# Kernel tuning notes

Measured on AMD Instinct MI355X. Metric: run time of the kernel, lower is better.

The kernel has to match this reference:

```python
import jax, jax.numpy as jnp
import numpy as np

N_NODES = 100000
N_EDGES = 800000
N_GRAPHS = 512
C_IN = 32
N_CLASSES = 10


def setup_inputs() -> dict:
    key = jax.random.key(0)
    ks = jax.random.split(key, 12)
    x = jax.random.normal(ks[0], (N_NODES, C_IN), dtype=jnp.float32)
    edge_index = jax.random.randint(ks[1], (2, N_EDGES), 0, N_NODES, dtype=jnp.int64)
    batch = jnp.sort(jax.random.randint(ks[2], (N_NODES,), 0, N_GRAPHS, dtype=jnp.int64))
    # GCNConv weights initialized ~ N(0, 1/sqrt(in_channels)) per the source
    W1 = jax.random.normal(ks[3], (C_IN, 64), dtype=jnp.float32) / np.sqrt(C_IN).astype(np.float32)
    bc1 = jnp.zeros((64,), jnp.float32)
    W2 = jax.random.normal(ks[4], (64, 128), dtype=jnp.float32) / np.sqrt(64).astype(np.float32)
    bc2 = jnp.zeros((128,), jnp.float32)
    W3 = jax.random.normal(ks[5], (128, 256), dtype=jnp.float32) / np.sqrt(128).astype(np.float32)
    bc3 = jnp.zeros((256,), jnp.float32)
    Wlin = jnp.full((256, N_CLASSES), 0.01, jnp.float32)  # lin.weight filled with 0.01
    blin = jnp.zeros((N_CLASSES,), jnp.float32)
    return dict(x=x, edge_index=edge_index, batch=batch,
                W1=W1, bc1=bc1, W2=W2, bc2=bc2, W3=W3, bc3=bc3,
                Wlin=Wlin, blin=blin)


def _gcn_conv(x, W, b, src, dst, n_nodes):
    """PyG GCNConv: symmetric-normalized aggregation with self-loops.
    out = D^{-1/2} (A + I) D^{-1/2} (x W) + b
    """
    h = x @ W  # [N, F_out]
    ones_e = jnp.ones(src.shape, h.dtype)
    deg = jax.ops.segment_sum(ones_e, dst, num_segments=n_nodes) + 1.0  # self-loop included
    dinv = jax.lax.rsqrt(deg)
    norm = dinv[src] * dinv[dst]  # [E]
    agg = jax.ops.segment_sum(h[src] * norm[:, None], dst, num_segments=n_nodes)
    # self-loop contribution: norm_ii = dinv_i^2
    return agg + h * (dinv * dinv)[:, None] + b


def reference(x, edge_index, batch, W1, bc1, W2, bc2, W3, bc3, Wlin, blin):
    src, dst = edge_index[0], edge_index[1]
    h = jax.nn.relu(_gcn_conv(x, W1, bc1, src, dst, N_NODES))
    h = jax.nn.relu(_gcn_conv(h, W2, bc2, src, dst, N_NODES))
    h = _gcn_conv(h, W3, bc3, src, dst, N_NODES)  # no relu before pooling (matches source)
    # global mean pool over graphs
    summed = jax.ops.segment_sum(h, batch, num_segments=N_GRAPHS)  # [G, 256]
    counts = jax.ops.segment_sum(jnp.ones((N_NODES, 1), h.dtype), batch, num_segments=N_GRAPHS)
    pooled = summed / jnp.clip(counts, 1.0)
    return pooled @ Wlin + blin  # [G, num_classes]
```

## Files before the change

kernel.cpp:

```cpp
#include <hip/hip_runtime.h>
#include <hip/hip_bf16.h>


#define NN 100000
#define NE 800000
#define NG 512
#define PARTS 4

typedef unsigned int u32;

__device__ __forceinline__ u32 pack_bf2(float lo, float hi) {
    u32 ul = __float_as_uint(lo);
    u32 uh = __float_as_uint(hi);
    ul = (ul + 0x7fffu + ((ul >> 16) & 1u)) >> 16;
    uh = (uh + 0x7fffu + ((uh >> 16) & 1u)) & 0xffff0000u;
    return uh | ul;
}

#define BF_FMA8(ACC, V, W_) do { \
    (ACC)[0] += __uint_as_float((V).x << 16) * (W_); \
    (ACC)[1] += __uint_as_float((V).x & 0xffff0000u) * (W_); \
    (ACC)[2] += __uint_as_float((V).y << 16) * (W_); \
    (ACC)[3] += __uint_as_float((V).y & 0xffff0000u) * (W_); \
    (ACC)[4] += __uint_as_float((V).z << 16) * (W_); \
    (ACC)[5] += __uint_as_float((V).z & 0xffff0000u) * (W_); \
    (ACC)[6] += __uint_as_float((V).w << 16) * (W_); \
    (ACC)[7] += __uint_as_float((V).w & 0xffff0000u) * (W_); \
} while (0)

#define FMA4(A, H, W_) do { (A).x += (H).x * (W_); (A).y += (H).y * (W_); \
                            (A).z += (H).z * (W_); (A).w += (H).w * (W_); } while (0)

__global__ __launch_bounds__(256) void deg_count(const int* __restrict__ dst,
                                                 int* __restrict__ deg, int nE) {
    int e = blockIdx.x * 256 + threadIdx.x;
    if (e < nE) atomicAdd(&deg[dst[e]], 1);
}

__global__ __launch_bounds__(256) void scanA(const int* __restrict__ deg,
                                             int* __restrict__ ex,
                                             int* __restrict__ bsum, int n) {
    __shared__ int sdata[256];
    const int t = threadIdx.x;
    const int base = blockIdx.x * 1024;
    const int idx = base + t * 4;
    int v[4];
#pragma unroll
    for (int k = 0; k < 4; ++k) v[k] = (idx + k < n) ? deg[idx + k] : 0;
    int ts = v[0] + v[1] + v[2] + v[3];
    sdata[t] = ts;
    __syncthreads();
    for (int off = 1; off < 256; off <<= 1) {
        int val = (t >= off) ? sdata[t - off] : 0;
        __syncthreads();
        sdata[t] += val;
        __syncthreads();
    }
    int run = sdata[t] - ts;
    if (t == 255) bsum[blockIdx.x] = sdata[255];
#pragma unroll
    for (int k = 0; k < 4; ++k) {
        if (idx + k < n) ex[idx + k] = run;
        run += v[k];
    }
}

__global__ __launch_bounds__(128) void scanB(int* __restrict__ bsum, int nb) {
    __shared__ int s[128];
    const int t = threadIdx.x;
    int orig = (t < nb) ? bsum[t] : 0;
    s[t] = orig;
    __syncthreads();
    for (int off = 1; off < 128; off <<= 1) {
        int val = (t >= off) ? s[t - off] : 0;
        __syncthreads();
        s[t] += val;
        __syncthreads();
    }
    if (t < nb) bsum[t] = s[t] - orig;
}

__global__ __launch_bounds__(256) void scanC(int* __restrict__ rp,
                                             const int* __restrict__ bsum,
                                             int* __restrict__ cursor,
                                             const int* __restrict__ deg,
                                             float* __restrict__ dinv,
                                             int n, int total) {
    int i = blockIdx.x * 256 + threadIdx.x;
    if (i < n) {
        int v = rp[i] + bsum[i >> 10];
        rp[i] = v;
        cursor[i] = v;
        dinv[i] = rsqrtf((float)deg[i] + 1.0f);
    }
    if (i == n) rp[n] = total;
}

__global__ __launch_bounds__(256) void fill_csr(const int* __restrict__ ei,
                                                const float* __restrict__ dinv,
                                                int* __restrict__ cursor,
                                                int2* __restrict__ cw, int nE) {
    int e = blockIdx.x * 256 + threadIdx.x;
    if (e >= nE) return;
    const int s = ei[e];
    const int d = ei[nE + e];
    const int pos = atomicAdd(&cursor[d], 1);
    const float wv = dinv[s] * dinv[d];
    cw[pos] = make_int2(s, __float_as_int(wv));
}

__global__ __launch_bounds__(256) void gather_gemm_l1(const float* __restrict__ X,
                                                      const int* __restrict__ rp,
                                                      const int2* __restrict__ cw,
                                                      const float* __restrict__ dinv,
                                                      const float* __restrict__ W,
                                                      const float* __restrict__ bias,
                                                      u32* __restrict__ out, int n) {
    constexpr int AS = 36;
    __shared__ float agg[32 * AS];
    __shared__ float Wl[32 * 64];
    float4 wr[2];
#pragma unroll
    for (int i = 0; i < 2; ++i)
        wr[i] = *reinterpret_cast<const float4*>(&W[(threadIdx.x + i * 256) * 4]);

    const int nl = threadIdx.x >> 3;
    const int j = (threadIdx.x & 7) * 4;
    const int node = blockIdx.x * 32 + nl;
    float4 a0 = make_float4(0.f, 0.f, 0.f, 0.f);
    float4 a1 = a0, a2 = a0, a3 = a0;
    if (node < n) {
        const float di = dinv[node];
        const float c = di * di;
        const float4 sv = *reinterpret_cast<const float4*>(&X[(long long)node * 32 + j]);
        FMA4(a0, sv, c);
        int e = rp[node];
        const int end = rp[node + 1];
        for (; e + 4 <= end; e += 4) {
            const int2 c0 = cw[e], c1 = cw[e + 1], c2 = cw[e + 2], c3 = cw[e + 3];
            const float4 h0 = *reinterpret_cast<const float4*>(&X[(long long)c0.x * 32 + j]);
            const float4 h1 = *reinterpret_cast<const float4*>(&X[(long long)c1.x * 32 + j]);
            const float4 h2 = *reinterpret_cast<const float4*>(&X[(long long)c2.x * 32 + j]);
            const float4 h3 = *reinterpret_cast<const float4*>(&X[(long long)c3.x * 32 + j]);
            FMA4(a0, h0, __int_as_float(c0.y));
            FMA4(a1, h1, __int_as_float(c1.y));
            FMA4(a2, h2, __int_as_float(c2.y));
            FMA4(a3, h3, __int_as_float(c3.y));
        }
        if (e + 2 <= end) {
            const int2 c0 = cw[e], c1 = cw[e + 1];
            const float4 h0 = *reinterpret_cast<const float4*>(&X[(long long)c0.x * 32 + j]);
            const float4 h1 = *reinterpret_cast<const float4*>(&X[(long long)c1.x * 32 + j]);
            FMA4(a0, h0, __int_as_float(c0.y));
            FMA4(a1, h1, __int_as_float(c1.y));
            e += 2;
        }
        if (e < end) {
            const int2 c0 = cw[e];
            const float4 h0 = *reinterpret_cast<const float4*>(&X[(long long)c0.x * 32 + j]);
            FMA4(a0, h0, __int_as_float(c0.y));
        }
        a0.x += a1.x + a2.x + a3.x; a0.y += a1.y + a2.y + a3.y;
        a0.z += a1.z + a2.z + a3.z; a0.w += a1.w + a2.w + a3.w;
    }
    *reinterpret_cast<float4*>(&agg[nl * AS + j]) = a0;
#pragma unroll
    for (int i = 0; i < 2; ++i)
        *reinterpret_cast<float4*>(&Wl[(threadIdx.x + i * 256) * 4]) = wr[i];
    __syncthreads();

    const int r0 = (threadIdx.x >> 4) * 2;
    const int cg = (threadIdx.x & 15) * 4;
    float4 o0 = make_float4(0.f, 0.f, 0.f, 0.f);
    float4 o1 = o0;
#pragma unroll 8
    for (int k = 0; k < 32; ++k) {
        const float4 wv = *reinterpret_cast<const float4*>(&Wl[k * 64 + cg]);
        const float x0 = agg[r0 * AS + k];
        const float x1 = agg[(r0 + 1) * AS + k];
        FMA4(o0, wv, x0);
        FMA4(o1, wv, x1);
    }
    const float4 bv = *reinterpret_cast<const float4*>(&bias[cg]);
    o0.x = fmaxf(o0.x + bv.x, 0.f); o0.y = fmaxf(o0.y + bv.y, 0.f);
    o0.z = fmaxf(o0.z + bv.z, 0.f); o0.w = fmaxf(o0.w + bv.w, 0.f);
    o1.x = fmaxf(o1.x + bv.x, 0.f); o1.y = fmaxf(o1.y + bv.y, 0.f);
    o1.z = fmaxf(o1.z + bv.z, 0.f); o1.w = fmaxf(o1.w + bv.w, 0.f);
    const int row0 = blockIdx.x * 32 + r0;
    if (row0 < n)
        *reinterpret_cast<uint2*>(&out[(long long)row0 * 32 + (cg >> 1)]) =
            make_uint2(pack_bf2(o0.x, o0.y), pack_bf2(o0.z, o0.w));
    if (row0 + 1 < n)
        *reinterpret_cast<uint2*>(&out[(long long)(row0 + 1) * 32 + (cg >> 1)]) =
            make_uint2(pack_bf2(o1.x, o1.y), pack_bf2(o1.z, o1.w));
}

__global__ __launch_bounds__(256) void gather_gemm_l2(const u32* __restrict__ X,
                                                      const int* __restrict__ rp,
                                                      const int2* __restrict__ cw,
                                                      const float* __restrict__ dinv,
                                                      const float* __restrict__ W,
                                                      const float* __restrict__ bias,
                                                      u32* __restrict__ out, int n) {
    constexpr int AS = 68;
    __shared__ float agg[32 * AS];
    __shared__ float Wl[64 * 128];
    float4 wr[8];
#pragma unroll
    for (int i = 0; i < 8; ++i)
        wr[i] = *reinterpret_cast<const float4*>(&W[(threadIdx.x + i * 256) * 4]);

    const int nl = threadIdx.x >> 3;
    const int j = threadIdx.x & 7;
    const int node = blockIdx.x * 32 + nl;
    float a0[8], a1[8], a2[8], a3[8];
#pragma unroll
    for (int q = 0; q < 8; ++q) { a0[q] = 0.f; a1[q] = 0.f; a2[q] = 0.f; a3[q] = 0.f; }
    if (node < n) {
        const float di = dinv[node];
        const float c = di * di;
        const uint4 sv = *reinterpret_cast<const uint4*>(&X[(long long)node * 32 + j * 4]);
        BF_FMA8(a0, sv, c);
        int e = rp[node];
        const int end = rp[node + 1];
        for (; e + 4 <= end; e += 4) {
            const int2 c0 = cw[e], c1 = cw[e + 1], c2 = cw[e + 2], c3 = cw[e + 3];
            const uint4 h0 = *reinterpret_cast<const uint4*>(&X[(long long)c0.x * 32 + j * 4]);
            const uint4 h1 = *reinterpret_cast<const uint4*>(&X[(long long)c1.x * 32 + j * 4]);
            const uint4 h2 = *reinterpret_cast<const uint4*>(&X[(long long)c2.x * 32 + j * 4]);
            const uint4 h3 = *reinterpret_cast<const uint4*>(&X[(long long)c3.x * 32 + j * 4]);
            BF_FMA8(a0, h0, __int_as_float(c0.y));
            BF_FMA8(a1, h1, __int_as_float(c1.y));
            BF_FMA8(a2, h2, __int_as_float(c2.y));
            BF_FMA8(a3, h3, __int_as_float(c3.y));
        }
        if (e + 2 <= end) {
            const int2 c0 = cw[e], c1 = cw[e + 1];
            const uint4 h0 = *reinterpret_cast<const uint4*>(&X[(long long)c0.x * 32 + j * 4]);
            const uint4 h1 = *reinterpret_cast<const uint4*>(&X[(long long)c1.x * 32 + j * 4]);
            BF_FMA8(a0, h0, __int_as_float(c0.y));
            BF_FMA8(a1, h1, __int_as_float(c1.y));
            e += 2;
        }
        if (e < end) {
            const int2 c0 = cw[e];
            const uint4 h0 = *reinterpret_cast<const uint4*>(&X[(long long)c0.x * 32 + j * 4]);
            BF_FMA8(a0, h0, __int_as_float(c0.y));
        }
#pragma unroll
        for (int q = 0; q < 8; ++q) a0[q] += a1[q] + a2[q] + a3[q];
    }
    *reinterpret_cast<float4*>(&agg[nl * AS + j * 8]) =
        make_float4(a0[0], a0[1], a0[2], a0[3]);
    *reinterpret_cast<float4*>(&agg[nl * AS + j * 8 + 4]) =
        make_float4(a0[4], a0[5], a0[6], a0[7]);
#pragma unroll
    for (int i = 0; i < 8; ++i)
        *reinterpret_cast<float4*>(&Wl[(threadIdx.x + i * 256) * 4]) = wr[i];
    __syncthreads();

    const int r0 = (threadIdx.x >> 5) * 4;
    const int cg = (threadIdx.x & 31) * 4;
    float4 o0 = make_float4(0.f, 0.f, 0.f, 0.f);
    float4 o1 = o0, o2 = o0, o3 = o0;
#pragma unroll 8
    for (int k = 0; k < 64; ++k) {
        const float4 wv = *reinterpret_cast<const float4*>(&Wl[k * 128 + cg]);
        const float x0 = agg[(r0 + 0) * AS + k];
        const float x1 = agg[(r0 + 1) * AS + k];
        const float x2 = agg[(r0 + 2) * AS + k];
        const float x3 = agg[(r0 + 3) * AS + k];
        FMA4(o0, wv, x0);
        FMA4(o1, wv, x1);
        FMA4(o2, wv, x2);
        FMA4(o3, wv, x3);
    }
    const float4 bv = *reinterpret_cast<const float4*>(&bias[cg]);
    const int row0 = blockIdx.x * 32 + r0;
    float4 oo[4] = {o0, o1, o2, o3};
#pragma unroll
    for (int r = 0; r < 4; ++r) {
        float4 o = oo[r];
        o.x = fmaxf(o.x + bv.x, 0.f); o.y = fmaxf(o.y + bv.y, 0.f);
        o.z = fmaxf(o.z + bv.z, 0.f); o.w = fmaxf(o.w + bv.w, 0.f);
        if (row0 + r < n)
            *reinterpret_cast<uint2*>(&out[(long long)(row0 + r) * 64 + (cg >> 1)]) =
                make_uint2(pack_bf2(o.x, o.y), pack_bf2(o.z, o.w));
    }
}

__device__ __forceinline__ int lower_bound_i(const int* __restrict__ a, int n, int key) {
    int lo = 0, hi = n;
    while (lo < hi) {
        int mid = (lo + hi) >> 1;
        if (a[mid] < key) lo = mid + 1; else hi = mid;
    }
    return lo;
}

__global__ __launch_bounds__(256) void gather_pool(const u32* __restrict__ H,
                                                   const int* __restrict__ rp,
                                                   const int2* __restrict__ cw,
                                                   const float* __restrict__ dinv,
                                                   const int* __restrict__ batch,
                                                   float* __restrict__ Spart, int n) {
    __shared__ float red[16 * 128];
    const int g = blockIdx.x / PARTS;
    const int part = blockIdx.x % PARTS;
    const int slot = threadIdx.x >> 4;
    const int j = threadIdx.x & 15;
    const int start = lower_bound_i(batch, n, g);
    const int end = lower_bound_i(batch, n, g + 1);
    float a0[8], a1[8], a2[8], a3[8];
#pragma unroll
    for (int q = 0; q < 8; ++q) { a0[q] = 0.f; a1[q] = 0.f; a2[q] = 0.f; a3[q] = 0.f; }
    for (int node = start + part * 16 + slot; node < end; node += PARTS * 16) {
        const float di = dinv[node];
        const float c = di * di;
        const uint4 sv = *reinterpret_cast<const uint4*>(&H[(long long)node * 64 + j * 4]);
        BF_FMA8(a0, sv, c);
        int e = rp[node];
        const int eend = rp[node + 1];
        for (; e + 4 <= eend; e += 4) {
            const int2 c0 = cw[e], c1 = cw[e + 1], c2 = cw[e + 2], c3 = cw[e + 3];
            const uint4 h0 = *reinterpret_cast<const uint4*>(&H[(long long)c0.x * 64 + j * 4]);
            const uint4 h1 = *reinterpret_cast<const uint4*>(&H[(long long)c1.x * 64 + j * 4]);
            const uint4 h2 = *reinterpret_cast<const uint4*>(&H[(long long)c2.x * 64 + j * 4]);
            const uint4 h3 = *reinterpret_cast<const uint4*>(&H[(long long)c3.x * 64 + j * 4]);
            BF_FMA8(a0, h0, __int_as_float(c0.y));
            BF_FMA8(a1, h1, __int_as_float(c1.y));
            BF_FMA8(a2, h2, __int_as_float(c2.y));
            BF_FMA8(a3, h3, __int_as_float(c3.y));
        }
        if (e + 2 <= eend) {
            const int2 c0 = cw[e], c1 = cw[e + 1];
            const uint4 h0 = *reinterpret_cast<const uint4*>(&H[(long long)c0.x * 64 + j * 4]);
            const uint4 h1 = *reinterpret_cast<const uint4*>(&H[(long long)c1.x * 64 + j * 4]);
            BF_FMA8(a0, h0, __int_as_float(c0.y));
            BF_FMA8(a1, h1, __int_as_float(c1.y));
            e += 2;
        }
        if (e < eend) {
            const int2 c0 = cw[e];
            const uint4 h0 = *reinterpret_cast<const uint4*>(&H[(long long)c0.x * 64 + j * 4]);
            BF_FMA8(a0, h0, __int_as_float(c0.y));
        }
    }
#pragma unroll
    for (int q = 0; q < 8; ++q) a0[q] += a1[q] + a2[q] + a3[q];
    *reinterpret_cast<float4*>(&red[slot * 128 + j * 8]) =
        make_float4(a0[0], a0[1], a0[2], a0[3]);
    *reinterpret_cast<float4*>(&red[slot * 128 + j * 8 + 4]) =
        make_float4(a0[4], a0[5], a0[6], a0[7]);
    __syncthreads();
    const int t = threadIdx.x;
    if (t < 128) {
        float s = 0.f;
#pragma unroll
        for (int sl = 0; sl < 16; ++sl) s += red[sl * 128 + t];
        Spart[(long long)blockIdx.x * 128 + t] = s;
    }
}

__global__ __launch_bounds__(256) void final_k(const float* __restrict__ Spart,
                                               const int* __restrict__ batch,
                                               const float* __restrict__ W3,
                                               const float* __restrict__ b3,
                                               const float* __restrict__ Wlin,
                                               const float* __restrict__ blin,
                                               float* __restrict__ out, int n) {
    __shared__ float srow[128];
    __shared__ float prow[256];
    const int g = blockIdx.x;
    const int t = threadIdx.x;
    if (t < 128) {
        float s = 0.f;
#pragma unroll
        for (int p = 0; p < PARTS; ++p)
            s += Spart[(long long)(g * PARTS + p) * 128 + t];
        srow[t] = s;
    }
    __syncthreads();
    const int start = lower_bound_i(batch, n, g);
    const int end = lower_bound_i(batch, n, g + 1);
    const float cnt = (float)(end - start);
    const float inv = 1.0f / fmaxf(cnt, 1.0f);
    const float bscale = cnt * inv;
    float p = 0.f;
    for (int k = 0; k < 128; ++k) p += srow[k] * W3[k * 256 + t];
    prow[t] = p * inv + b3[t] * bscale;
    __syncthreads();
    if (t < 10) {
        float a = blin[t];
        for (int f = 0; f < 256; ++f) a += prow[f] * Wlin[f * 10 + t];
        out[g * 10 + t] = a;
    }
}

extern "C" void kernel_launch(void* const* d_in, const int* in_sizes, int n_in,
                              void* d_out, int out_size, void* d_ws, size_t ws_size,
                              hipStream_t stream) {
    const float* x     = (const float*)d_in[0];
    const int*   ei    = (const int*)d_in[1];
    const int*   batch = (const int*)d_in[2];
    const float* W1    = (const float*)d_in[3];
    const float* bc1   = (const float*)d_in[4];
    const float* W2    = (const float*)d_in[5];
    const float* bc2   = (const float*)d_in[6];
    const float* W3    = (const float*)d_in[7];
    const float* bc3   = (const float*)d_in[8];
    const float* Wlin  = (const float*)d_in[9];
    const float* blin  = (const float*)d_in[10];
    float* out = (float*)d_out;

    char* w = (char*)d_ws;
    int*   deg    = (int*)w;               w += 131072 * 4;
    int*   rp     = (int*)w;               w += 131072 * 4;
    int*   cursor = (int*)w;               w += 131072 * 4;
    int*   bsum   = (int*)w;               w += 256 * 4;
    float* dinv   = (float*)w;             w += 131072 * 4;
    int2*  cw     = (int2*)w;              w += (long long)NE * 8;
    u32*   Q      = (u32*)w;               w += (long long)NN * 64 * 2;
    u32*   P      = (u32*)w;               w += (long long)NN * 128 * 2;
    float* Spart  = (float*)w;             w += (long long)NG * PARTS * 128 * 4;

    const int nbScanA = (NN + 1023) / 1024;

    hipMemsetAsync(deg, 0, NN * sizeof(int), stream);
    deg_count<<<(NE + 255) / 256, 256, 0, stream>>>(ei + NE, deg, NE);
    scanA<<<nbScanA, 256, 0, stream>>>(deg, rp, bsum, NN);
    scanB<<<1, 128, 0, stream>>>(bsum, nbScanA);
    scanC<<<(NN + 256) / 256, 256, 0, stream>>>(rp, bsum, cursor, deg, dinv, NN, NE);
    fill_csr<<<(NE + 255) / 256, 256, 0, stream>>>(ei, dinv, cursor, cw, NE);

    gather_gemm_l1<<<(NN + 31) / 32, 256, 0, stream>>>(x, rp, cw, dinv, W1, bc1, Q, NN);
    gather_gemm_l2<<<(NN + 31) / 32, 256, 0, stream>>>(Q, rp, cw, dinv, W2, bc2, P, NN);
    gather_pool<<<NG * PARTS, 256, 0, stream>>>(P, rp, cw, dinv, batch, Spart, NN);
    final_k<<<NG, 256, 0, stream>>>(Spart, batch, W3, bc3, Wlin, blin, out, NN);
}
```

Baseline: 225.4 us.

## Cast input features to bf16 before layer-1 gather and raise pool partitions

Adds a kernel that converts the fp32 input features to packed bf16. The layer-1 gather then reads 8-byte bf16 rows per lane instead of 16-byte fp32 rows, halving the random-gather traffic for that layer. It also doubles PARTS for the pooling kernel, which gives it more blocks and parallelism but produces more partial sums for the final reduction. The cost is an extra conversion pass over x and bf16 rounding error on the input features.

```diff
diff --git a/kernel.cpp b/kernel.cpp
--- a/kernel.cpp
+++ b/kernel.cpp
@@ -5,7 +5,7 @@
 #define NN 100000
 #define NE 800000
 #define NG 512
-#define PARTS 4
+#define PARTS 8
 
 typedef unsigned int u32;
 
@@ -28,8 +28,24 @@
     (ACC)[7] += __uint_as_float((V).w & 0xffff0000u) * (W_); \
 } while (0)
 
+#define BF_FMA4(ACC, V, W_) do { \
+    (ACC)[0] += __uint_as_float((V).x << 16) * (W_); \
+    (ACC)[1] += __uint_as_float((V).x & 0xffff0000u) * (W_); \
+    (ACC)[2] += __uint_as_float((V).y << 16) * (W_); \
+    (ACC)[3] += __uint_as_float((V).y & 0xffff0000u) * (W_); \
+} while (0)
+
 #define FMA4(A, H, W_) do { (A).x += (H).x * (W_); (A).y += (H).y * (W_); \
                             (A).z += (H).z * (W_); (A).w += (H).w * (W_); } while (0)
+
+__global__ __launch_bounds__(256) void xcast(const float* __restrict__ x,
+                                             u32* __restrict__ xb, int n4) {
+    int i = blockIdx.x * 256 + threadIdx.x;
+    if (i >= n4) return;
+    const float4 v = *reinterpret_cast<const float4*>(&x[i * 4]);
+    *reinterpret_cast<uint2*>(&xb[i * 2]) =
+        make_uint2(pack_bf2(v.x, v.y), pack_bf2(v.z, v.w));
+}
 
 __global__ __launch_bounds__(256) void deg_count(const int* __restrict__ dst,
                                                  int* __restrict__ deg, int nE) {
@@ -109,7 +125,7 @@
     cw[pos] = make_int2(s, __float_as_int(wv));
 }
 
-__global__ __launch_bounds__(256) void gather_gemm_l1(const float* __restrict__ X,
+__global__ __launch_bounds__(256) void gather_gemm_l1(const u32* __restrict__ X,
                                                       const int* __restrict__ rp,
                                                       const int2* __restrict__ cw,
                                                       const float* __restrict__ dinv,
@@ -125,45 +141,47 @@
         wr[i] = *reinterpret_cast<const float4*>(&W[(threadIdx.x + i * 256) * 4]);
 
     const int nl = threadIdx.x >> 3;
-    const int j = (threadIdx.x & 7) * 4;
+    const int j = threadIdx.x & 7;
     const int node = blockIdx.x * 32 + nl;
-    float4 a0 = make_float4(0.f, 0.f, 0.f, 0.f);
-    float4 a1 = a0, a2 = a0, a3 = a0;
+    float a0[4], a1[4], a2[4], a3[4];
+#pragma unroll
+    for (int q = 0; q < 4; ++q) { a0[q] = 0.f; a1[q] = 0.f; a2[q] = 0.f; a3[q] = 0.f; }
     if (node < n) {
         const float di = dinv[node];
         const float c = di * di;
-        const float4 sv = *reinterpret_cast<const float4*>(&X[(long long)node * 32 + j]);
-        FMA4(a0, sv, c);
+        const uint2 sv = *reinterpret_cast<const uint2*>(&X[(long long)node * 16 + j * 2]);
+        BF_FMA4(a0, sv, c);
         int e = rp[node];
         const int end = rp[node + 1];
         for (; e + 4 <= end; e += 4) {
             const int2 c0 = cw[e], c1 = cw[e + 1], c2 = cw[e + 2], c3 = cw[e + 3];
-            const float4 h0 = *reinterpret_cast<const float4*>(&X[(long long)c0.x * 32 + j]);
-            const float4 h1 = *reinterpret_cast<const float4*>(&X[(long long)c1.x * 32 + j]);
-            const float4 h2 = *reinterpret_cast<const float4*>(&X[(long long)c2.x * 32 + j]);
-            const float4 h3 = *reinterpret_cast<const float4*>(&X[(long long)c3.x * 32 + j]);
-            FMA4(a0, h0, __int_as_float(c0.y));
-            FMA4(a1, h1, __int_as_float(c1.y));
-            FMA4(a2, h2, __int_as_float(c2.y));
-            FMA4(a3, h3, __int_as_float(c3.y));
+            const uint2 h0 = *reinterpret_cast<const uint2*>(&X[(long long)c0.x * 16 + j * 2]);
+            const uint2 h1 = *reinterpret_cast<const uint2*>(&X[(long long)c1.x * 16 + j * 2]);
+            const uint2 h2 = *reinterpret_cast<const uint2*>(&X[(long long)c2.x * 16 + j * 2]);
+            const uint2 h3 = *reinterpret_cast<const uint2*>(&X[(long long)c3.x * 16 + j * 2]);
+            BF_FMA4(a0, h0, __int_as_float(c0.y));
+            BF_FMA4(a1, h1, __int_as_float(c1.y));
+            BF_FMA4(a2, h2, __int_as_float(c2.y));
+            BF_FMA4(a3, h3, __int_as_float(c3.y));
         }
         if (e + 2 <= end) {
             const int2 c0 = cw[e], c1 = cw[e + 1];
-            const float4 h0 = *reinterpret_cast<const float4*>(&X[(long long)c0.x * 32 + j]);
-            const float4 h1 = *reinterpret_cast<const float4*>(&X[(long long)c1.x * 32 + j]);
-            FMA4(a0, h0, __int_as_float(c0.y));
-            FMA4(a1, h1, __int_as_float(c1.y));
+            const uint2 h0 = *reinterpret_cast<const uint2*>(&X[(long long)c0.x * 16 + j * 2]);
+            const uint2 h1 = *reinterpret_cast<const uint2*>(&X[(long long)c1.x * 16 + j * 2]);
+            BF_FMA4(a0, h0, __int_as_float(c0.y));
+            BF_FMA4(a1, h1, __int_as_float(c1.y));
             e += 2;
         }
         if (e < end) {
             const int2 c0 = cw[e];
-            const float4 h0 = *reinterpret_cast<const float4*>(&X[(long long)c0.x * 32 + j]);
-            FMA4(a0, h0, __int_as_float(c0.y));
-        }
-        a0.x += a1.x + a2.x + a3.x; a0.y += a1.y + a2.y + a3.y;
-        a0.z += a1.z + a2.z + a3.z; a0.w += a1.w + a2.w + a3.w;
-    }
-    *reinterpret_cast<float4*>(&agg[nl * AS + j]) = a0;
+            const uint2 h0 = *reinterpret_cast<const uint2*>(&X[(long long)c0.x * 16 + j * 2]);
+            BF_FMA4(a0, h0, __int_as_float(c0.y));
+        }
+#pragma unroll
+        for (int q = 0; q < 4; ++q) a0[q] += a1[q] + a2[q] + a3[q];
+    }
+    *reinterpret_cast<float4*>(&agg[nl * AS + j * 4]) =
+        make_float4(a0[0], a0[1], a0[2], a0[3]);
 #pragma unroll
     for (int i = 0; i < 2; ++i)
         *reinterpret_cast<float4*>(&Wl[(threadIdx.x + i * 256) * 4]) = wr[i];
@@ -420,20 +438,22 @@
     int*   bsum   = (int*)w;               w += 256 * 4;
     float* dinv   = (float*)w;             w += 131072 * 4;
     int2*  cw     = (int2*)w;              w += (long long)NE * 8;
-    u32*   Q      = (u32*)w;               w += (long long)NN * 64 * 2;
-    u32*   P      = (u32*)w;               w += (long long)NN * 128 * 2;
+    u32*   xb     = (u32*)w;               w += (long long)NN * 16 * 4;
+    u32*   Q      = (u32*)w;               w += (long long)NN * 32 * 4;
+    u32*   P      = (u32*)w;               w += (long long)NN * 64 * 4;
     float* Spart  = (float*)w;             w += (long long)NG * PARTS * 128 * 4;
 
     const int nbScanA = (NN + 1023) / 1024;
 
     hipMemsetAsync(deg, 0, NN * sizeof(int), stream);
+    xcast<<<(NN * 8 + 255) / 256, 256, 0, stream>>>(x, xb, NN * 8);
     deg_count<<<(NE + 255) / 256, 256, 0, stream>>>(ei + NE, deg, NE);
     scanA<<<nbScanA, 256, 0, stream>>>(deg, rp, bsum, NN);
     scanB<<<1, 128, 0, stream>>>(bsum, nbScanA);
     scanC<<<(NN + 256) / 256, 256, 0, stream>>>(rp, bsum, cursor, deg, dinv, NN, NE);
     fill_csr<<<(NE + 255) / 256, 256, 0, stream>>>(ei, dinv, cursor, cw, NE);
 
-    gather_gemm_l1<<<(NN + 31) / 32, 256, 0, stream>>>(x, rp, cw, dinv, W1, bc1, Q, NN);
+    gather_gemm_l1<<<(NN + 31) / 32, 256, 0, stream>>>(xb, rp, cw, dinv, W1, bc1, Q, NN);
     gather_gemm_l2<<<(NN + 31) / 32, 256, 0, stream>>>(Q, rp, cw, dinv, W2, bc2, P, NN);
     gather_pool<<<NG * PARTS, 256, 0, stream>>>(P, rp, cw, dinv, batch, Spart, NN);
     final_k<<<NG, 256, 0, stream>>>(Spart, batch, W3, bc3, Wlin, blin, out, NN);
```

New measurement: 238.9 us. +6.0%, slower.
